# Kernel tuning notes

Hardware: AMD Instinct MI355X
Metric: run time of the kernel (lower is better)

Reference implementation:

```python
import jax, jax.numpy as jnp
import numpy as np

B, S, D, E = 8, 2048, 1024, 8


def setup_inputs() -> dict:
    key = jax.random.key(0)
    k1, k2, k3, k4 = jax.random.split(key, 4)
    return {
        "x": jax.random.normal(k1, (B, S, D), dtype=jnp.float32),
        "routing_scores": jax.random.normal(k2, (B, E), dtype=jnp.float32),
        "expert_w": jax.random.normal(k3, (E, D, D), dtype=jnp.float32) / np.sqrt(D),
        "expert_b": jax.random.normal(k4, (E, D), dtype=jnp.float32),
        "k": 2,
    }


def reference(x, routing_scores, expert_w, expert_b, k):
    batch = routing_scores.shape[0]
    # top-k gating mask + renormalization scale (torch.topk + scatter_ equivalent)
    values, indices = jax.lax.top_k(routing_scores, k)              # (B, k)
    mask = jnp.zeros_like(routing_scores, dtype=bool)
    mask = mask.at[jnp.arange(batch)[:, None], indices].set(True)    # (B, E)
    scale = 1.0 / (values.sum(axis=1, keepdims=True) + 1e-8)         # (B, 1)
    masked_scores = scale * routing_scores * mask                    # (B, E)

    # dense per-expert transform: expert_e(x) = x @ W_e + b_e  -> (E, B, S, D)
    expert_out = jnp.einsum("bsd,edf->ebsf", x, expert_w) + expert_b[:, None, None, :]
    # weighted scatter-accumulate over experts (zero weight for inactive pairs)
    final_output = jnp.einsum("be,ebsf->bsf", masked_scores, expert_out)

    return final_output, mask.sum(axis=0)
```

## Files before the change

### kernel.cpp

```cpp
#include <hip/hip_runtime.h>

#define NB 8
#define NS 2048
#define ND 1024
#define NE 8

typedef unsigned short ushort_t;
typedef __attribute__((ext_vector_type(8))) short bf16x8;
typedef __attribute__((ext_vector_type(4))) float f32x4;

__device__ __forceinline__ unsigned short f2bf(float f) {
    union { float f; unsigned int u; } x; x.f = f;
    unsigned int u = x.u + 0x7fffu + ((x.u >> 16) & 1u);
    return (unsigned short)(u >> 16);
}

__device__ __forceinline__ void gload16(const void* g, void* l) {
    __builtin_amdgcn_global_load_lds(
        (const __attribute__((address_space(1))) unsigned int*)g,
        (__attribute__((address_space(3))) unsigned int*)l, 16, 0, 0);
}

__device__ __forceinline__ void coef_local(const float* __restrict__ scores,
                                           int b, int k, float* cf) {
    float s[NE];
#pragma unroll
    for (int e = 0; e < NE; ++e) s[e] = scores[b * NE + e];
    bool sel[NE];
#pragma unroll
    for (int e = 0; e < NE; ++e) sel[e] = false;
    float sum = 0.f;
    for (int j = 0; j < k; ++j) {
        int best = 0; float bv = -3.4e38f;
#pragma unroll
        for (int e = 0; e < NE; ++e)
            if (!sel[e] && s[e] > bv) { bv = s[e]; best = e; }
        sel[best] = true; sum += bv;
    }
    float scale = 1.f / (sum + 1e-8f);
#pragma unroll
    for (int e = 0; e < NE; ++e) cf[e] = sel[e] ? scale * s[e] : 0.f;
}

__global__ void prep_kernel(const float* __restrict__ x,
                            const float* __restrict__ scores,
                            const float* __restrict__ W,
                            const float* __restrict__ eb,
                            const int* __restrict__ kp,
                            ushort_t* __restrict__ xb,
                            ushort_t* __restrict__ wct,
                            float* __restrict__ bias,
                            float* __restrict__ counts) {
    __shared__ float tile[64][65];
    __shared__ int selS[NB][NE];
    int bid = blockIdx.x;
    int t = threadIdx.x;

    if (bid < 2048) {
        int b = bid >> 8;
        int f0 = (bid & 15) * 64, d0 = ((bid >> 4) & 15) * 64;
        float cf[NE];
        coef_local(scores, b, kp[0], cf);
        int lr = t >> 4;
        int lc = (t & 15) * 4;
        float4 acc[4];
#pragma unroll
        for (int it = 0; it < 4; ++it) acc[it] = make_float4(0.f, 0.f, 0.f, 0.f);
#pragma unroll
        for (int e = 0; e < NE; ++e) {
            float c = cf[e];
            if (c != 0.f) {
                const float* We = W + ((size_t)e * ND * ND);
#pragma unroll
                for (int it = 0; it < 4; ++it) {
                    int d = d0 + lr + it * 16;
                    float4 v = *(const float4*)(We + (size_t)d * ND + f0 + lc);
                    acc[it].x += c * v.x; acc[it].y += c * v.y;
                    acc[it].z += c * v.z; acc[it].w += c * v.w;
                }
            }
        }
#pragma unroll
        for (int it = 0; it < 4; ++it) {
            int r = lr + it * 16;
            tile[r][lc + 0] = acc[it].x; tile[r][lc + 1] = acc[it].y;
            tile[r][lc + 2] = acc[it].z; tile[r][lc + 3] = acc[it].w;
        }
        __syncthreads();
        int dl = t & 63;
        int frow = t >> 6;
        ushort_t* dst = wct + (size_t)b * ND * ND + (size_t)f0 * ND + d0 + dl;
#pragma unroll
        for (int it = 0; it < 16; ++it) {
            int f = frow + it * 4;
            dst[(size_t)f * ND] = f2bf(tile[dl][f]);
        }
    } else if (bid < 10240) {
        size_t i = (size_t)(bid - 2048) * 256 + t;
        const float4* p = (const float4*)x + 2 * i;
        float4 a = p[0], b = p[1];
        uint4 o;
        o.x = (unsigned)f2bf(a.x) | ((unsigned)f2bf(a.y) << 16);
        o.y = (unsigned)f2bf(a.z) | ((unsigned)f2bf(a.w) << 16);
        o.z = (unsigned)f2bf(b.x) | ((unsigned)f2bf(b.y) << 16);
        o.w = (unsigned)f2bf(b.z) | ((unsigned)f2bf(b.w) << 16);
        ((uint4*)xb)[i] = o;
    } else if (bid < 10272) {
        int i = bid - 10240;
        int b = i >> 2, f = (i & 3) * 256 + t;
        float cf[NE];
        coef_local(scores, b, kp[0], cf);
        float acc = 0.f;
#pragma unroll
        for (int e = 0; e < NE; ++e)
            if (cf[e] != 0.f) acc += cf[e] * eb[e * ND + f];
        bias[b * ND + f] = acc;
    } else {
        int k = kp[0];
        if (t < NB) {
            float s[NE];
#pragma unroll
            for (int e = 0; e < NE; ++e) s[e] = scores[t * NE + e];
            bool sel[NE];
#pragma unroll
            for (int e = 0; e < NE; ++e) sel[e] = false;
            for (int j = 0; j < k; ++j) {
                int best = 0; float bv = -3.4e38f;
#pragma unroll
                for (int e = 0; e < NE; ++e)
                    if (!sel[e] && s[e] > bv) { bv = s[e]; best = e; }
                sel[best] = true;
            }
#pragma unroll
            for (int e = 0; e < NE; ++e) selS[t][e] = sel[e] ? 1 : 0;
        }
        __syncthreads();
        if (t < NE) {
            int c = 0;
#pragma unroll
            for (int b = 0; b < NB; ++b) c += selS[b][t];
            counts[t] = (float)c;
        }
    }
}

__global__ __launch_bounds__(512, 4) void gemm_kernel(const ushort_t* __restrict__ xb,
                                                      const ushort_t* __restrict__ wct,
                                                      const float* __restrict__ bias,
                                                      float* __restrict__ out) {
    __shared__ ushort_t ldsA[3][256 * 32];
    __shared__ ushort_t ldsB[3][128 * 32];

    int bid = blockIdx.x;
    int b = bid & 7;
    int tile = bid >> 3;
    int m0 = (tile >> 3) * 256;
    int n0 = (tile & 7) * 128;
    const ushort_t* A  = xb  + ((size_t)b * NS * ND) + (size_t)m0 * ND;
    const ushort_t* Bt = wct + ((size_t)b * ND * ND) + (size_t)n0 * ND;

    int t = threadIdx.x, lane = t & 63, wave = t >> 6;
    int wm = wave >> 1, wn = wave & 1;
    int fr = lane & 15, fq = lane >> 4;

    int srow = t >> 2;
    int slotg = (t & 3) ^ ((srow >> 1) & 3);
    const ushort_t* sA = A  + (size_t)srow * ND + slotg * 8;
    const ushort_t* sB = Bt + (size_t)srow * ND + slotg * 8;
    int ldst = t * 8;

    int swzb = (fq ^ ((fr >> 1) & 3)) * 16;
    int aoff[4], boff[4];
#pragma unroll
    for (int mi = 0; mi < 4; ++mi) aoff[mi] = (wm * 64 + mi * 16 + fr) * 64 + swzb;
#pragma unroll
    for (int nj = 0; nj < 4; ++nj) boff[nj] = (wn * 64 + nj * 16 + fr) * 64 + swzb;

    f32x4 acc[4][4];
#pragma unroll
    for (int i = 0; i < 4; ++i)
#pragma unroll
        for (int j = 0; j < 4; ++j) acc[i][j] = (f32x4){0.f, 0.f, 0.f, 0.f};

    const int NT = ND / 32;

#define STAGE(kt, buf) do { \
    gload16(sA + (kt) * 32,            &ldsA[buf][ldst]); \
    gload16(sA + (kt) * 32 + 128 * ND, &ldsA[buf][4096 + ldst]); \
    gload16(sB + (kt) * 32,            &ldsB[buf][ldst]); \
} while (0)

    STAGE(0, 0);
    STAGE(1, 1);
    asm volatile("s_waitcnt vmcnt(3)" ::: "memory");
    __builtin_amdgcn_s_barrier();

    int cur = 0;
    for (int kt = 0; kt < NT; ++kt) {
        const char* lA = (const char*)&ldsA[cur][0];
        const char* lB = (const char*)&ldsB[cur][0];
        int sq = cur + 2; if (sq >= 3) sq -= 3;

        __builtin_amdgcn_sched_barrier(0);
        bf16x8 af[4], bf[4];
#pragma unroll
        for (int nj = 0; nj < 4; ++nj) bf[nj] = *(const bf16x8*)(lB + boff[nj]);
#pragma unroll
        for (int mi = 0; mi < 4; ++mi) af[mi] = *(const bf16x8*)(lA + aoff[mi]);
        if (kt + 2 < NT) STAGE(kt + 2, sq);
        __builtin_amdgcn_sched_barrier(0);
        asm volatile("s_waitcnt lgkmcnt(0)" ::: "memory");
        __builtin_amdgcn_sched_barrier(0);
        __builtin_amdgcn_s_setprio(1);
#pragma unroll
        for (int mi = 0; mi < 4; ++mi)
#pragma unroll
            for (int nj = 0; nj < 4; ++nj)
                acc[mi][nj] = __builtin_amdgcn_mfma_f32_16x16x32_bf16(af[mi], bf[nj], acc[mi][nj], 0, 0, 0);
        __builtin_amdgcn_s_setprio(0);
        __builtin_amdgcn_sched_barrier(0);
        if (kt + 2 < NT) {
            asm volatile("s_waitcnt vmcnt(3)" ::: "memory");
        } else if (kt + 1 < NT) {
            asm volatile("s_waitcnt vmcnt(0)" ::: "memory");
        }
        if (kt + 1 < NT) __builtin_amdgcn_s_barrier();
        cur += 1; if (cur == 3) cur = 0;
    }

#undef STAGE

    const float* bs = bias + b * ND;
    float* O = out + ((size_t)b * NS * ND);
#pragma unroll
    for (int mi = 0; mi < 4; ++mi) {
        int row = m0 + wm * 64 + mi * 16 + fq * 4;
#pragma unroll
        for (int nj = 0; nj < 4; ++nj) {
            int col = n0 + wn * 64 + nj * 16 + fr;
            float bv = bs[col];
            f32x4 v = acc[mi][nj];
#pragma unroll
            for (int r = 0; r < 4; ++r)
                O[(size_t)(row + r) * ND + col] = v[r] + bv;
        }
    }
}

extern "C" void kernel_launch(void* const* d_in, const int* in_sizes, int n_in,
                              void* d_out, int out_size, void* d_ws, size_t ws_size,
                              hipStream_t stream) {
    const float* x      = (const float*)d_in[0];
    const float* scores = (const float*)d_in[1];
    const float* Wx     = (const float*)d_in[2];
    const float* eb     = (const float*)d_in[3];
    const int*   kp     = (const int*)d_in[4];
    float* out = (float*)d_out;
    char* ws = (char*)d_ws;

    float*    bias  = (float*)(ws + 1024);
    ushort_t* xbuf  = (ushort_t*)(ws + 65536);
    ushort_t* wct   = (ushort_t*)(ws + 65536 + (size_t)NB * NS * ND * 2);
    float*    counts = out + (size_t)NB * NS * ND;

    prep_kernel<<<10273, 256, 0, stream>>>(x, scores, Wx, eb, kp, xbuf, wct, bias, counts);
    gemm_kernel<<<512, 512, 0, stream>>>(xbuf, wct, bias, out);
}
```

Before: 67.53 us.

## Shrink GEMM block tile to 128x128 with 256 threads and double buffering

Reduces each GEMM workgroup from a 256x128 output tile with 8 waves to a 128x128 tile with 4 waves, doubling the grid to 1024 blocks. The LDS pipeline drops from triple to double buffering: the next K-slice is prefetched at the top of each iteration and fully drained with vmcnt(0) before the barrier. The intent is better load balance across CUs and lower LDS use per block. In exchange, each loaded A/B byte is reused less, and the shallower pipeline hides global-load latency less well.

```diff
diff --git a/kernel.cpp b/kernel.cpp
--- a/kernel.cpp
+++ b/kernel.cpp
@@ -144,17 +144,17 @@
     }
 }
 
-__global__ __launch_bounds__(512, 4) void gemm_kernel(const ushort_t* __restrict__ xb,
+__global__ __launch_bounds__(256, 4) void gemm_kernel(const ushort_t* __restrict__ xb,
                                                       const ushort_t* __restrict__ wct,
                                                       const float* __restrict__ bias,
                                                       float* __restrict__ out) {
-    __shared__ ushort_t ldsA[3][256 * 32];
-    __shared__ ushort_t ldsB[3][128 * 32];
+    __shared__ ushort_t ldsA[2][128 * 32];
+    __shared__ ushort_t ldsB[2][128 * 32];
 
     int bid = blockIdx.x;
     int b = bid & 7;
     int tile = bid >> 3;
-    int m0 = (tile >> 3) * 256;
+    int m0 = (tile >> 3) * 128;
     int n0 = (tile & 7) * 128;
     const ushort_t* A  = xb  + ((size_t)b * NS * ND) + (size_t)m0 * ND;
     const ushort_t* Bt = wct + ((size_t)b * ND * ND) + (size_t)n0 * ND;
@@ -165,8 +165,10 @@
 
     int srow = t >> 2;
     int slotg = (t & 3) ^ ((srow >> 1) & 3);
-    const ushort_t* sA = A  + (size_t)srow * ND + slotg * 8;
-    const ushort_t* sB = Bt + (size_t)srow * ND + slotg * 8;
+    const ushort_t* sA0 = A  + (size_t)srow * ND + slotg * 8;
+    const ushort_t* sA1 = A  + (size_t)(srow + 64) * ND + slotg * 8;
+    const ushort_t* sB0 = Bt + (size_t)srow * ND + slotg * 8;
+    const ushort_t* sB1 = Bt + (size_t)(srow + 64) * ND + slotg * 8;
     int ldst = t * 8;
 
     int swzb = (fq ^ ((fr >> 1) & 3)) * 16;
@@ -185,30 +187,29 @@
     const int NT = ND / 32;
 
 #define STAGE(kt, buf) do { \
-    gload16(sA + (kt) * 32,            &ldsA[buf][ldst]); \
-    gload16(sA + (kt) * 32 + 128 * ND, &ldsA[buf][4096 + ldst]); \
-    gload16(sB + (kt) * 32,            &ldsB[buf][ldst]); \
+    gload16(sA0 + (kt) * 32, &ldsA[buf][ldst]); \
+    gload16(sA1 + (kt) * 32, &ldsA[buf][2048 + ldst]); \
+    gload16(sB0 + (kt) * 32, &ldsB[buf][ldst]); \
+    gload16(sB1 + (kt) * 32, &ldsB[buf][2048 + ldst]); \
 } while (0)
 
     STAGE(0, 0);
-    STAGE(1, 1);
-    asm volatile("s_waitcnt vmcnt(3)" ::: "memory");
+    asm volatile("s_waitcnt vmcnt(0)" ::: "memory");
     __builtin_amdgcn_s_barrier();
 
-    int cur = 0;
     for (int kt = 0; kt < NT; ++kt) {
+        int cur = kt & 1;
+        bool pre = (kt + 1 < NT);
         const char* lA = (const char*)&ldsA[cur][0];
         const char* lB = (const char*)&ldsB[cur][0];
-        int sq = cur + 2; if (sq >= 3) sq -= 3;
-
-        __builtin_amdgcn_sched_barrier(0);
+
+        if (pre) STAGE(kt + 1, cur ^ 1);
+
         bf16x8 af[4], bf[4];
 #pragma unroll
         for (int nj = 0; nj < 4; ++nj) bf[nj] = *(const bf16x8*)(lB + boff[nj]);
 #pragma unroll
         for (int mi = 0; mi < 4; ++mi) af[mi] = *(const bf16x8*)(lA + aoff[mi]);
-        if (kt + 2 < NT) STAGE(kt + 2, sq);
-        __builtin_amdgcn_sched_barrier(0);
         asm volatile("s_waitcnt lgkmcnt(0)" ::: "memory");
         __builtin_amdgcn_sched_barrier(0);
         __builtin_amdgcn_s_setprio(1);
@@ -218,14 +219,10 @@
             for (int nj = 0; nj < 4; ++nj)
                 acc[mi][nj] = __builtin_amdgcn_mfma_f32_16x16x32_bf16(af[mi], bf[nj], acc[mi][nj], 0, 0, 0);
         __builtin_amdgcn_s_setprio(0);
-        __builtin_amdgcn_sched_barrier(0);
-        if (kt + 2 < NT) {
-            asm volatile("s_waitcnt vmcnt(3)" ::: "memory");
-        } else if (kt + 1 < NT) {
+        if (pre) {
             asm volatile("s_waitcnt vmcnt(0)" ::: "memory");
-        }
-        if (kt + 1 < NT) __builtin_amdgcn_s_barrier();
-        cur += 1; if (cur == 3) cur = 0;
+            __builtin_amdgcn_s_barrier();
+        }
     }
 
 #undef STAGE
@@ -264,5 +261,5 @@
     float*    counts = out + (size_t)NB * NS * ND;
 
     prep_kernel<<<10273, 256, 0, stream>>>(x, scores, Wx, eb, kp, xbuf, wct, bias, counts);
-    gemm_kernel<<<512, 512, 0, stream>>>(xbuf, wct, bias, out);
-}
+    gemm_kernel<<<1024, 256, 0, stream>>>(xbuf, wct, bias, out);
+}
```

Result: slower. 70.69 us (+4.7%).

## Fuse fp32-to-bf16 conversion of x into GEMM A-tile loading

Applied to the files above, without the earlier changes.

Removes the separate prep pass that converted x to bf16 in a workspace buffer. The GEMM now loads fp32 x into registers, converts to bf16 and writes swizzled tiles into LDS, while B still uses direct global-to-LDS loads. This is meant to eliminate a full write and re-read of the converted activation. The cost is double the A-load bytes per tile, register pressure, and a restructured wait/barrier pipeline.

```diff
diff --git a/kernel.cpp b/kernel.cpp
--- a/kernel.cpp
+++ b/kernel.cpp
@@ -15,6 +15,10 @@
     return (unsigned short)(u >> 16);
 }
 
+__device__ __forceinline__ unsigned pk2(float a, float b) {
+    return (unsigned)f2bf(a) | ((unsigned)f2bf(b) << 16);
+}
+
 __device__ __forceinline__ void gload16(const void* g, void* l) {
     __builtin_amdgcn_global_load_lds(
         (const __attribute__((address_space(1))) unsigned int*)g,
@@ -42,12 +46,10 @@
     for (int e = 0; e < NE; ++e) cf[e] = sel[e] ? scale * s[e] : 0.f;
 }
 
-__global__ void prep_kernel(const float* __restrict__ x,
-                            const float* __restrict__ scores,
+__global__ void prep_kernel(const float* __restrict__ scores,
                             const float* __restrict__ W,
                             const float* __restrict__ eb,
                             const int* __restrict__ kp,
-                            ushort_t* __restrict__ xb,
                             ushort_t* __restrict__ wct,
                             float* __restrict__ bias,
                             float* __restrict__ counts) {
@@ -95,18 +97,8 @@
             int f = frow + it * 4;
             dst[(size_t)f * ND] = f2bf(tile[dl][f]);
         }
-    } else if (bid < 10240) {
-        size_t i = (size_t)(bid - 2048) * 256 + t;
-        const float4* p = (const float4*)x + 2 * i;
-        float4 a = p[0], b = p[1];
-        uint4 o;
-        o.x = (unsigned)f2bf(a.x) | ((unsigned)f2bf(a.y) << 16);
-        o.y = (unsigned)f2bf(a.z) | ((unsigned)f2bf(a.w) << 16);
-        o.z = (unsigned)f2bf(b.x) | ((unsigned)f2bf(b.y) << 16);
-        o.w = (unsigned)f2bf(b.z) | ((unsigned)f2bf(b.w) << 16);
-        ((uint4*)xb)[i] = o;
-    } else if (bid < 10272) {
-        int i = bid - 10240;
+    } else if (bid < 2080) {
+        int i = bid - 2048;
         int b = i >> 2, f = (i & 3) * 256 + t;
         float cf[NE];
         coef_local(scores, b, kp[0], cf);
@@ -144,7 +136,7 @@
     }
 }
 
-__global__ __launch_bounds__(512, 4) void gemm_kernel(const ushort_t* __restrict__ xb,
+__global__ __launch_bounds__(512, 4) void gemm_kernel(const float* __restrict__ x,
                                                       const ushort_t* __restrict__ wct,
                                                       const float* __restrict__ bias,
                                                       float* __restrict__ out) {
@@ -156,7 +148,6 @@
     int tile = bid >> 3;
     int m0 = (tile >> 3) * 256;
     int n0 = (tile & 7) * 128;
-    const ushort_t* A  = xb  + ((size_t)b * NS * ND) + (size_t)m0 * ND;
     const ushort_t* Bt = wct + ((size_t)b * ND * ND) + (size_t)n0 * ND;
 
     int t = threadIdx.x, lane = t & 63, wave = t >> 6;
@@ -165,9 +156,14 @@
 
     int srow = t >> 2;
     int slotg = (t & 3) ^ ((srow >> 1) & 3);
-    const ushort_t* sA = A  + (size_t)srow * ND + slotg * 8;
     const ushort_t* sB = Bt + (size_t)srow * ND + slotg * 8;
-    int ldst = t * 8;
+    int ldstB = t * 8;
+
+    int ar = t >> 1, ah = t & 1;
+    const float* xA = x + ((size_t)b * NS * ND) + (size_t)(m0 + ar) * ND + ah * 16;
+    int swA = (ar >> 1) & 3;
+    int woff0 = ar * 32 + ((2 * ah) ^ swA) * 8;
+    int woff1 = ar * 32 + ((2 * ah + 1) ^ swA) * 8;
 
     int swzb = (fq ^ ((fr >> 1) & 3)) * 16;
     int aoff[4], boff[4];
@@ -184,30 +180,46 @@
 
     const int NT = ND / 32;
 
-#define STAGE(kt, buf) do { \
-    gload16(sA + (kt) * 32,            &ldsA[buf][ldst]); \
-    gload16(sA + (kt) * 32 + 128 * ND, &ldsA[buf][4096 + ldst]); \
-    gload16(sB + (kt) * 32,            &ldsB[buf][ldst]); \
+    float4 rA0, rA1, rA2, rA3;
+#define LOAD_A(kt) do { \
+    const float* xp = xA + (kt) * 32; \
+    rA0 = *(const float4*)(xp);      rA1 = *(const float4*)(xp + 4); \
+    rA2 = *(const float4*)(xp + 8);  rA3 = *(const float4*)(xp + 12); \
 } while (0)
-
-    STAGE(0, 0);
-    STAGE(1, 1);
-    asm volatile("s_waitcnt vmcnt(3)" ::: "memory");
+#define CVT_WRITE(buf) do { \
+    uint4 o0, o1; \
+    o0.x = pk2(rA0.x, rA0.y); o0.y = pk2(rA0.z, rA0.w); \
+    o0.z = pk2(rA1.x, rA1.y); o0.w = pk2(rA1.z, rA1.w); \
+    o1.x = pk2(rA2.x, rA2.y); o1.y = pk2(rA2.z, rA2.w); \
+    o1.z = pk2(rA3.x, rA3.y); o1.w = pk2(rA3.z, rA3.w); \
+    *(uint4*)(&ldsA[buf][woff0]) = o0; \
+    *(uint4*)(&ldsA[buf][woff1]) = o1; \
+} while (0)
+
+    LOAD_A(0);
+    gload16(sB, &ldsB[0][ldstB]);
+    gload16(sB + 32, &ldsB[1][ldstB]);
+    asm volatile("s_waitcnt vmcnt(2)" ::: "memory");
+    CVT_WRITE(0);
+    LOAD_A(1);
+    asm volatile("s_waitcnt vmcnt(5)" ::: "memory");
+    asm volatile("s_waitcnt lgkmcnt(0)" ::: "memory");
     __builtin_amdgcn_s_barrier();
 
-    int cur = 0;
     for (int kt = 0; kt < NT; ++kt) {
+        int cur = kt; while (cur >= 3) cur -= 3;
         const char* lA = (const char*)&ldsA[cur][0];
         const char* lB = (const char*)&ldsB[cur][0];
+        int nb = cur + 1; if (nb == 3) nb = 0;
         int sq = cur + 2; if (sq >= 3) sq -= 3;
 
-        __builtin_amdgcn_sched_barrier(0);
+        if (kt + 2 < NT) gload16(sB + (kt + 2) * 32, &ldsB[sq][ldstB]);
+
         bf16x8 af[4], bf[4];
 #pragma unroll
         for (int nj = 0; nj < 4; ++nj) bf[nj] = *(const bf16x8*)(lB + boff[nj]);
 #pragma unroll
         for (int mi = 0; mi < 4; ++mi) af[mi] = *(const bf16x8*)(lA + aoff[mi]);
-        if (kt + 2 < NT) STAGE(kt + 2, sq);
         __builtin_amdgcn_sched_barrier(0);
         asm volatile("s_waitcnt lgkmcnt(0)" ::: "memory");
         __builtin_amdgcn_sched_barrier(0);
@@ -219,16 +231,21 @@
                 acc[mi][nj] = __builtin_amdgcn_mfma_f32_16x16x32_bf16(af[mi], bf[nj], acc[mi][nj], 0, 0, 0);
         __builtin_amdgcn_s_setprio(0);
         __builtin_amdgcn_sched_barrier(0);
-        if (kt + 2 < NT) {
-            asm volatile("s_waitcnt vmcnt(3)" ::: "memory");
-        } else if (kt + 1 < NT) {
-            asm volatile("s_waitcnt vmcnt(0)" ::: "memory");
-        }
-        if (kt + 1 < NT) __builtin_amdgcn_s_barrier();
-        cur += 1; if (cur == 3) cur = 0;
-    }
-
-#undef STAGE
+
+        if (kt + 1 < NT) {
+            if (kt + 2 < NT) asm volatile("s_waitcnt vmcnt(1)" ::: "memory");
+            else             asm volatile("s_waitcnt vmcnt(0)" ::: "memory");
+            __builtin_amdgcn_sched_barrier(0);
+            CVT_WRITE(nb);
+            if (kt + 2 < NT) LOAD_A(kt + 2);
+            __builtin_amdgcn_sched_barrier(0);
+            asm volatile("s_waitcnt lgkmcnt(0)" ::: "memory");
+            __builtin_amdgcn_s_barrier();
+        }
+    }
+
+#undef LOAD_A
+#undef CVT_WRITE
 
     const float* bs = bias + b * ND;
     float* O = out + ((size_t)b * NS * ND);
@@ -259,10 +276,9 @@
     char* ws = (char*)d_ws;
 
     float*    bias  = (float*)(ws + 1024);
-    ushort_t* xbuf  = (ushort_t*)(ws + 65536);
-    ushort_t* wct   = (ushort_t*)(ws + 65536 + (size_t)NB * NS * ND * 2);
+    ushort_t* wct   = (ushort_t*)(ws + 65536);
     float*    counts = out + (size_t)NB * NS * ND;
 
-    prep_kernel<<<10273, 256, 0, stream>>>(x, scores, Wx, eb, kp, xbuf, wct, bias, counts);
-    gemm_kernel<<<512, 512, 0, stream>>>(xbuf, wct, bias, out);
-}
+    prep_kernel<<<2081, 256, 0, stream>>>(scores, Wx, eb, kp, wct, bias, counts);
+    gemm_kernel<<<512, 512, 0, stream>>>(x, wct, bias, out);
+}
```

Result: slower. 74.31 us (+10.0%).
